# Performance work log

Hardware: AMD Instinct MI355X
Metric: run time of the kernel (lower is better)

## Reference

```python
import jax, jax.numpy as jnp
import numpy as np

T, M, D_IN, N = 4096, 512, 11, 51


def setup_inputs() -> dict:
    key = jax.random.key(0)
    ks = jax.random.split(key, 11)
    s = 1.0 / np.sqrt(N)  # torch LSTMCell/Linear default init scale
    return {
        "input": jax.random.normal(ks[0], (T, M, D_IN), dtype=jnp.float32),
        "W_ih1": jax.random.uniform(ks[1], (4 * N, D_IN), jnp.float32, -s, s),
        "W_hh1": jax.random.uniform(ks[2], (4 * N, N), jnp.float32, -s, s),
        "b_ih1": jax.random.uniform(ks[3], (4 * N,), jnp.float32, -s, s),
        "b_hh1": jax.random.uniform(ks[4], (4 * N,), jnp.float32, -s, s),
        "W_ih2": jax.random.uniform(ks[5], (4 * N, N), jnp.float32, -s, s),
        "W_hh2": jax.random.uniform(ks[6], (4 * N, N), jnp.float32, -s, s),
        "b_ih2": jax.random.uniform(ks[7], (4 * N,), jnp.float32, -s, s),
        "b_hh2": jax.random.uniform(ks[8], (4 * N,), jnp.float32, -s, s),
        "W_lin": jax.random.uniform(ks[9], (1, N), jnp.float32, -s, s),
        "b_lin": jax.random.uniform(ks[10], (1,), jnp.float32, -s, s),
        "future": 0,
    }


def _lstm_cell(x, h, c, W_ih, W_hh, b_ih, b_hh):
    # torch gate order: input, forget, cell(g), output
    gates = x @ W_ih.T + b_ih + h @ W_hh.T + b_hh  # [m, 4n]
    i, f, g, o = jnp.split(gates, 4, axis=-1)
    c_new = jax.nn.sigmoid(f) * c + jax.nn.sigmoid(i) * jnp.tanh(g)
    h_new = jax.nn.sigmoid(o) * jnp.tanh(c_new)
    return h_new, c_new


def reference(input, W_ih1, W_hh1, b_ih1, b_hh1, W_ih2, W_hh2, b_ih2, b_hh2,
              W_lin, b_lin, future):
    m = input.shape[1]
    n = W_hh1.shape[1]
    h1 = jnp.zeros((m, n), jnp.float32)
    c1 = jnp.zeros((m, n), jnp.float32)
    h2 = jnp.zeros((m, n), jnp.float32)
    c2 = jnp.zeros((m, n), jnp.float32)

    def step(carry, x_t):
        h1, c1, h2, c2 = carry
        h1, c1 = _lstm_cell(x_t, h1, c1, W_ih1, W_hh1, b_ih1, b_hh1)
        h2, c2 = _lstm_cell(h1, h2, c2, W_ih2, W_hh2, b_ih2, b_hh2)
        out = h2 @ W_lin.T + b_lin  # [m, 1]
        return (h1, c1, h2, c2), out

    _, outs = jax.lax.scan(step, (h1, c1, h2, c2), input)  # [T, m, 1]
    # torch.stack(outputs, 1).squeeze(2) -> [m, T]
    # (future loop is dimensionally invalid in the original for future>0; future=0)
    return outs[:, :, 0].T
```

## Files before the change

### kernel.cpp

```cpp
#include <hip/hip_runtime.h>

#define T_STEPS 4096
#define M_BATCH 512
#define D_INP   11
#define N_HID   51
#define G4      204

typedef float v4f __attribute__((ext_vector_type(4)));

__device__ __forceinline__ float tanh_fast(float v) {
    return 2.0f * __builtin_amdgcn_rcpf(1.0f + __expf(-2.0f * v)) - 1.0f;
}

__attribute__((amdgpu_waves_per_eu(2, 2)))
__global__ __launch_bounds__(256)
void lstm2_pipe2(const float* __restrict__ input,
                 const float* __restrict__ W_ih1, const float* __restrict__ W_hh1,
                 const float* __restrict__ b_ih1, const float* __restrict__ b_hh1,
                 const float* __restrict__ W_ih2, const float* __restrict__ W_hh2,
                 const float* __restrict__ b_ih2, const float* __restrict__ b_hh2,
                 const float* __restrict__ W_lin, const float* __restrict__ b_lin,
                 float* __restrict__ out)
{
    const int  tid = threadIdx.x;
    const int  col = blockIdx.x;
    const bool isg = tid < G4;
    const int  j   = isg ? tid : 0;

    __shared__ __align__(16) float hbuf[4][52];
    __shared__ __align__(16) float xs[2][64 * 12];
    __shared__ float act1[208];
    __shared__ float act2[208];
    __shared__ float outbuf[128];

    v4f wi1v[3], wh1v[13], wi2v[13], wh2v[13];
    #pragma unroll
    for (int i = 0; i < 3; ++i)
        #pragma unroll
        for (int e = 0; e < 4; ++e) {
            int k = i * 4 + e;
            wi1v[i][e] = (k < D_INP) ? W_ih1[j * D_INP + k] : 0.f;
        }
    #pragma unroll
    for (int i = 0; i < 13; ++i)
        #pragma unroll
        for (int e = 0; e < 4; ++e) {
            int k = i * 4 + e;
            float w1 = (k < N_HID) ? W_hh1[j * N_HID + k] : 0.f;
            float w2 = (k < N_HID) ? W_ih2[j * N_HID + k] : 0.f;
            float w3 = (k < N_HID) ? W_hh2[j * N_HID + k] : 0.f;
            wh1v[i][e] = w1; wi2v[i][e] = w2; wh2v[i][e] = w3;
        }
    const float bias1 = isg ? (b_ih1[j] + b_hh1[j]) : 0.f;
    const float bias2 = isg ? (b_ih2[j] + b_hh2[j]) : 0.f;
    const bool  gg = (j >= 2 * N_HID) && (j < 3 * N_HID);
    const float Sa = gg ? 2.f : 1.f, Aa = gg ? 2.f : 1.f, Ba = gg ? -1.f : 0.f;

    const int   u2   = tid - 64;
    const float wlin = (tid >= 64 && tid < 64 + N_HID) ? W_lin[u2] : 0.f;
    const float blin = b_lin[0];
    float c1 = 0.f, c2 = 0.f;

    if (tid < 208) (&hbuf[0][0])[tid] = 0.f;
    { float* xf = &xs[0][0];
      for (int i = tid; i < 2 * 64 * 12; i += 256) xf[i] = 0.f; }

    auto xload = [&](int c, int e) -> float {
        int s = e / 11, d = e - s * 11;
        int tc = c * 64 + s; if (tc > T_STEPS - 1) tc = T_STEPS - 1;
        return input[((size_t)tc * M_BATCH + col) * D_INP + d];
    };
    auto xput = [&](int buf, int e, float v) {
        int s = e / 11, d = e - s * 11;
        xs[buf][s * 12 + d] = v;
    };
    __syncthreads();

    {
        float v0 = xload(0, tid);
        float v1 = xload(0, tid + 256);
        float v2 = (tid < 192) ? xload(0, tid + 512) : 0.f;
        xput(0, tid, v0);
        xput(0, tid + 256, v1);
        if (tid < 192) xput(0, tid + 512, v2);
    }
    __syncthreads();

    float xr0 = 0.f, xr1 = 0.f, xr2 = 0.f;

    for (int t = 0; t <= T_STEPS; ++t) {
        if ((t & 63) == 0) {
            const int c = (t >> 6) + 1;
            xr0 = xload(c, tid);
            xr1 = xload(c, tid + 256);
            if (tid < 192) xr2 = xload(c, tid + 512);
        }
        if (isg) {
            const v4f* xp  = (const v4f*)&xs[(t >> 6) & 1][(t & 63) * 12];
            const v4f* h1p = (const v4f*)hbuf[(t + 1) & 1];
            const v4f* h2p = (const v4f*)hbuf[2 + (t & 1)];

            v4f a0 = xp[0] * wi1v[0];
            v4f a1 = xp[1] * wi1v[1];
            a0 += xp[2] * wi1v[2];
            v4f b0 = {0.f, 0.f, 0.f, 0.f}, b1 = {0.f, 0.f, 0.f, 0.f};
            #pragma unroll
            for (int i = 0; i < 13; ++i) {
                v4f h = h1p[i];
                if (i & 1) { a1 += h * wh1v[i]; b1 += h * wi2v[i]; }
                else       { a0 += h * wh1v[i]; b0 += h * wi2v[i]; }
            }
            #pragma unroll
            for (int i = 0; i < 13; ++i) {
                v4f h = h2p[i];
                if (i & 1) b1 += h * wh2v[i];
                else       b0 += h * wh2v[i];
            }
            v4f as = a0 + a1;
            float g1 = (as.x + as.y) + (as.z + as.w) + bias1;
            act1[j] = Aa * __builtin_amdgcn_rcpf(1.f + __expf(-Sa * g1)) + Ba;
            v4f bs = b0 + b1;
            float g2 = (bs.x + bs.y) + (bs.z + bs.w) + bias2;
            act2[j] = Aa * __builtin_amdgcn_rcpf(1.f + __expf(-Sa * g2)) + Ba;
        }
        __syncthreads();

        if (tid < N_HID) {
            float iv = act1[tid],             fv = act1[N_HID + tid];
            float gv = act1[2 * N_HID + tid], ov = act1[3 * N_HID + tid];
            c1 = fv * c1 + iv * gv;
            hbuf[t & 1][tid] = ov * tanh_fast(c1);
        }
        if (tid >= 64 && tid < 128) {
            float part = 0.f;
            if (u2 < N_HID && t >= 1) {
                float iv = act2[u2],             fv = act2[N_HID + u2];
                float gv = act2[2 * N_HID + u2], ov = act2[3 * N_HID + u2];
                c2 = fv * c2 + iv * gv;
                float h2v = ov * tanh_fast(c2);
                hbuf[2 + ((t - 1) & 1)][u2] = h2v;
                part = wlin * h2v;
            }
            #pragma unroll
            for (int off = 32; off > 0; off >>= 1)
                part += __shfl_down(part, off, 64);
            if (u2 == 0 && t >= 1) outbuf[(t - 1) & 127] = part + blin;
        }
        if ((t & 63) == 32) {
            const int buf = ((t >> 6) + 1) & 1;
            xput(buf, tid, xr0);
            xput(buf, tid + 256, xr1);
            if (tid < 192) xput(buf, tid + 512, xr2);
        }
        if ((t & 63) == 1 && t >= 65 && tid >= 128 && tid < 192) {
            const int tb = (t - 65) + (tid - 128);
            out[(size_t)col * T_STEPS + tb] = outbuf[tb & 127];
        }
        __syncthreads();
    }

    if (tid >= 128 && tid < 192) {
        const int idx = 4032 + (tid - 128);
        out[(size_t)col * T_STEPS + idx] = outbuf[idx & 127];
    }
}

extern "C" void kernel_launch(void* const* d_in, const int* in_sizes, int n_in,
                              void* d_out, int out_size, void* d_ws, size_t ws_size,
                              hipStream_t stream) {
    const float* input = (const float*)d_in[0];
    const float* W_ih1 = (const float*)d_in[1];
    const float* W_hh1 = (const float*)d_in[2];
    const float* b_ih1 = (const float*)d_in[3];
    const float* b_hh1 = (const float*)d_in[4];
    const float* W_ih2 = (const float*)d_in[5];
    const float* W_hh2 = (const float*)d_in[6];
    const float* b_ih2 = (const float*)d_in[7];
    const float* b_hh2 = (const float*)d_in[8];
    const float* W_lin = (const float*)d_in[9];
    const float* b_lin = (const float*)d_in[10];
    float* out = (float*)d_out;

    lstm2_pipe2<<<M_BATCH, 256, 0, stream>>>(
        input, W_ih1, W_hh1, b_ih1, b_hh1,
        W_ih2, W_hh2, b_ih2, b_hh2, W_lin, b_lin, out);
}
```

Baseline: 4.461 ms.

## Specialize waves per layer and keep all four gates per lane in registers

Each block now uses two waves, one per LSTM layer. Each lane holds the four gate weight rows for its hidden unit in 104 vector registers, so it computes the gate preactivations, activations and cell update itself. This removes the act1/act2 shared-memory round trip and one of the two barriers per timestep. The cost is much higher register pressure (waves_per_eu 1) and sequential work per lane across four gates, which lengthens the per-step critical path.

Measured after the change: 7.974 ms. 1.79x slower.

```diff
diff --git a/kernel.cpp b/kernel.cpp
--- a/kernel.cpp
+++ b/kernel.cpp
@@ -4,66 +4,85 @@
 #define M_BATCH 512
 #define D_INP   11
 #define N_HID   51
-#define G4      204
 
 typedef float v4f __attribute__((ext_vector_type(4)));
 
+__device__ __forceinline__ float sigmoid_fast(float v) {
+    return __builtin_amdgcn_rcpf(1.0f + __expf(-v));
+}
 __device__ __forceinline__ float tanh_fast(float v) {
     return 2.0f * __builtin_amdgcn_rcpf(1.0f + __expf(-2.0f * v)) - 1.0f;
 }
 
-__attribute__((amdgpu_waves_per_eu(2, 2)))
-__global__ __launch_bounds__(256)
-void lstm2_pipe2(const float* __restrict__ input,
-                 const float* __restrict__ W_ih1, const float* __restrict__ W_hh1,
-                 const float* __restrict__ b_ih1, const float* __restrict__ b_hh1,
-                 const float* __restrict__ W_ih2, const float* __restrict__ W_hh2,
-                 const float* __restrict__ b_ih2, const float* __restrict__ b_hh2,
-                 const float* __restrict__ W_lin, const float* __restrict__ b_lin,
-                 float* __restrict__ out)
+__attribute__((amdgpu_waves_per_eu(1, 1)))
+__global__ __launch_bounds__(128)
+void lstm2_wavespec(const float* __restrict__ input,
+                    const float* __restrict__ W_ih1, const float* __restrict__ W_hh1,
+                    const float* __restrict__ b_ih1, const float* __restrict__ b_hh1,
+                    const float* __restrict__ W_ih2, const float* __restrict__ W_hh2,
+                    const float* __restrict__ b_ih2, const float* __restrict__ b_hh2,
+                    const float* __restrict__ W_lin, const float* __restrict__ b_lin,
+                    float* __restrict__ out)
 {
-    const int  tid = threadIdx.x;
-    const int  col = blockIdx.x;
-    const bool isg = tid < G4;
-    const int  j   = isg ? tid : 0;
-
-    __shared__ __align__(16) float hbuf[4][52];
+    const int  tid  = threadIdx.x;
+    const int  col  = blockIdx.x;
+    const int  wid  = tid >> 6;
+    const int  lane = tid & 63;
+    const bool valid = lane < N_HID;
+
+    __shared__ __align__(16) float hbuf[2][52];
+    __shared__ __align__(16) float h2buf[52];
     __shared__ __align__(16) float xs[2][64 * 12];
-    __shared__ float act1[208];
-    __shared__ float act2[208];
     __shared__ float outbuf[128];
 
-    v4f wi1v[3], wh1v[13], wi2v[13], wh2v[13];
-    #pragma unroll
-    for (int i = 0; i < 3; ++i)
+    v4f   wv[104];
+    float bias[4];
+    float wlin = 0.f;
+    const float blin = b_lin[0];
+    float cstate = 0.f;
+
+    if (wid == 0) {
         #pragma unroll
-        for (int e = 0; e < 4; ++e) {
-            int k = i * 4 + e;
-            wi1v[i][e] = (k < D_INP) ? W_ih1[j * D_INP + k] : 0.f;
-        }
-    #pragma unroll
-    for (int i = 0; i < 13; ++i)
+        for (int q = 0; q < 4; ++q) {
+            const int r = q * N_HID + lane;
+            bias[q] = valid ? (b_ih1[r] + b_hh1[r]) : 0.f;
+            #pragma unroll
+            for (int i = 0; i < 3; ++i)
+                #pragma unroll
+                for (int e = 0; e < 4; ++e) {
+                    const int k = 4 * i + e;
+                    wv[i * 4 + q][e] = (valid && k < D_INP) ? W_ih1[r * D_INP + k] : 0.f;
+                }
+            #pragma unroll
+            for (int i = 3; i < 16; ++i)
+                #pragma unroll
+                for (int e = 0; e < 4; ++e) {
+                    const int k = 4 * (i - 3) + e;
+                    wv[i * 4 + q][e] = (valid && k < N_HID) ? W_hh1[r * N_HID + k] : 0.f;
+                }
+        }
+    } else {
         #pragma unroll
-        for (int e = 0; e < 4; ++e) {
-            int k = i * 4 + e;
-            float w1 = (k < N_HID) ? W_hh1[j * N_HID + k] : 0.f;
-            float w2 = (k < N_HID) ? W_ih2[j * N_HID + k] : 0.f;
-            float w3 = (k < N_HID) ? W_hh2[j * N_HID + k] : 0.f;
-            wh1v[i][e] = w1; wi2v[i][e] = w2; wh2v[i][e] = w3;
-        }
-    const float bias1 = isg ? (b_ih1[j] + b_hh1[j]) : 0.f;
-    const float bias2 = isg ? (b_ih2[j] + b_hh2[j]) : 0.f;
-    const bool  gg = (j >= 2 * N_HID) && (j < 3 * N_HID);
-    const float Sa = gg ? 2.f : 1.f, Aa = gg ? 2.f : 1.f, Ba = gg ? -1.f : 0.f;
-
-    const int   u2   = tid - 64;
-    const float wlin = (tid >= 64 && tid < 64 + N_HID) ? W_lin[u2] : 0.f;
-    const float blin = b_lin[0];
-    float c1 = 0.f, c2 = 0.f;
-
-    if (tid < 208) (&hbuf[0][0])[tid] = 0.f;
-    { float* xf = &xs[0][0];
-      for (int i = tid; i < 2 * 64 * 12; i += 256) xf[i] = 0.f; }
+        for (int q = 0; q < 4; ++q) {
+            const int r = q * N_HID + lane;
+            bias[q] = valid ? (b_ih2[r] + b_hh2[r]) : 0.f;
+            #pragma unroll
+            for (int i = 0; i < 13; ++i)
+                #pragma unroll
+                for (int e = 0; e < 4; ++e) {
+                    const int k = 4 * i + e;
+                    wv[i * 4 + q][e] = (valid && k < N_HID) ? W_ih2[r * N_HID + k] : 0.f;
+                }
+            #pragma unroll
+            for (int i = 13; i < 26; ++i)
+                #pragma unroll
+                for (int e = 0; e < 4; ++e) {
+                    const int k = 4 * (i - 13) + e;
+                    wv[i * 4 + q][e] = (valid && k < N_HID) ? W_hh2[r * N_HID + k] : 0.f;
+                }
+        }
+        wlin = valid ? W_lin[lane] : 0.f;
+    }
 
     auto xload = [&](int c, int e) -> float {
         int s = e / 11, d = e - s * 11;
@@ -74,93 +93,104 @@
         int s = e / 11, d = e - s * 11;
         xs[buf][s * 12 + d] = v;
     };
+
+    for (int i = tid; i < 2 * 52; i += 128) (&hbuf[0][0])[i] = 0.f;
+    for (int i = tid; i < 52;     i += 128) h2buf[i] = 0.f;
+    for (int i = tid; i < 2 * 64 * 12; i += 128) (&xs[0][0])[i] = 0.f;
     __syncthreads();
-
-    {
-        float v0 = xload(0, tid);
-        float v1 = xload(0, tid + 256);
-        float v2 = (tid < 192) ? xload(0, tid + 512) : 0.f;
-        xput(0, tid, v0);
-        xput(0, tid + 256, v1);
-        if (tid < 192) xput(0, tid + 512, v2);
+    #pragma unroll
+    for (int i = 0; i < 6; ++i) {
+        const int e = tid + 128 * i;
+        if (e < 704) xput(0, e, xload(0, e));
     }
     __syncthreads();
 
-    float xr0 = 0.f, xr1 = 0.f, xr2 = 0.f;
-
+    float xr[6];
+
+    #pragma unroll 1
     for (int t = 0; t <= T_STEPS; ++t) {
         if ((t & 63) == 0) {
             const int c = (t >> 6) + 1;
-            xr0 = xload(c, tid);
-            xr1 = xload(c, tid + 256);
-            if (tid < 192) xr2 = xload(c, tid + 512);
-        }
-        if (isg) {
-            const v4f* xp  = (const v4f*)&xs[(t >> 6) & 1][(t & 63) * 12];
-            const v4f* h1p = (const v4f*)hbuf[(t + 1) & 1];
-            const v4f* h2p = (const v4f*)hbuf[2 + (t & 1)];
-
-            v4f a0 = xp[0] * wi1v[0];
-            v4f a1 = xp[1] * wi1v[1];
-            a0 += xp[2] * wi1v[2];
-            v4f b0 = {0.f, 0.f, 0.f, 0.f}, b1 = {0.f, 0.f, 0.f, 0.f};
+            #pragma unroll
+            for (int i = 0; i < 6; ++i) {
+                const int e = tid + 128 * i;
+                xr[i] = (e < 704) ? xload(c, e) : 0.f;
+            }
+        }
+
+        const v4f* h1p = (const v4f*)hbuf[(t + 1) & 1];
+        v4f acc0 = {0.f,0.f,0.f,0.f}, acc1 = acc0, acc2 = acc0, acc3 = acc0;
+
+        if (wid == 0) {
+            const v4f* xp = (const v4f*)&xs[(t >> 6) & 1][(t & 63) * 12];
+            #pragma unroll
+            for (int i = 0; i < 3; ++i) {
+                const v4f v = xp[i];
+                acc0 += v * wv[i * 4 + 0]; acc1 += v * wv[i * 4 + 1];
+                acc2 += v * wv[i * 4 + 2]; acc3 += v * wv[i * 4 + 3];
+            }
+            #pragma unroll
+            for (int i = 3; i < 16; ++i) {
+                const v4f h = h1p[i - 3];
+                acc0 += h * wv[i * 4 + 0]; acc1 += h * wv[i * 4 + 1];
+                acc2 += h * wv[i * 4 + 2]; acc3 += h * wv[i * 4 + 3];
+            }
+        } else {
+            const v4f* h2p = (const v4f*)h2buf;
             #pragma unroll
             for (int i = 0; i < 13; ++i) {
-                v4f h = h1p[i];
-                if (i & 1) { a1 += h * wh1v[i]; b1 += h * wi2v[i]; }
-                else       { a0 += h * wh1v[i]; b0 += h * wi2v[i]; }
-            }
-            #pragma unroll
-            for (int i = 0; i < 13; ++i) {
-                v4f h = h2p[i];
-                if (i & 1) b1 += h * wh2v[i];
-                else       b0 += h * wh2v[i];
-            }
-            v4f as = a0 + a1;
-            float g1 = (as.x + as.y) + (as.z + as.w) + bias1;
-            act1[j] = Aa * __builtin_amdgcn_rcpf(1.f + __expf(-Sa * g1)) + Ba;
-            v4f bs = b0 + b1;
-            float g2 = (bs.x + bs.y) + (bs.z + bs.w) + bias2;
-            act2[j] = Aa * __builtin_amdgcn_rcpf(1.f + __expf(-Sa * g2)) + Ba;
-        }
-        __syncthreads();
-
-        if (tid < N_HID) {
-            float iv = act1[tid],             fv = act1[N_HID + tid];
-            float gv = act1[2 * N_HID + tid], ov = act1[3 * N_HID + tid];
-            c1 = fv * c1 + iv * gv;
-            hbuf[t & 1][tid] = ov * tanh_fast(c1);
-        }
-        if (tid >= 64 && tid < 128) {
-            float part = 0.f;
-            if (u2 < N_HID && t >= 1) {
-                float iv = act2[u2],             fv = act2[N_HID + u2];
-                float gv = act2[2 * N_HID + u2], ov = act2[3 * N_HID + u2];
-                c2 = fv * c2 + iv * gv;
-                float h2v = ov * tanh_fast(c2);
-                hbuf[2 + ((t - 1) & 1)][u2] = h2v;
-                part = wlin * h2v;
-            }
+                const v4f h = h1p[i];
+                acc0 += h * wv[i * 4 + 0]; acc1 += h * wv[i * 4 + 1];
+                acc2 += h * wv[i * 4 + 2]; acc3 += h * wv[i * 4 + 3];
+            }
+            #pragma unroll
+            for (int i = 13; i < 26; ++i) {
+                const v4f h = h2p[i - 13];
+                acc0 += h * wv[i * 4 + 0]; acc1 += h * wv[i * 4 + 1];
+                acc2 += h * wv[i * 4 + 2]; acc3 += h * wv[i * 4 + 3];
+            }
+        }
+
+        const float pre0 = (acc0.x + acc0.y) + (acc0.z + acc0.w) + bias[0];
+        const float pre1 = (acc1.x + acc1.y) + (acc1.z + acc1.w) + bias[1];
+        const float pre2 = (acc2.x + acc2.y) + (acc2.z + acc2.w) + bias[2];
+        const float pre3 = (acc3.x + acc3.y) + (acc3.z + acc3.w) + bias[3];
+        const float iv = sigmoid_fast(pre0);
+        const float fv = sigmoid_fast(pre1);
+        const float gv = tanh_fast(pre2);
+        const float ov = sigmoid_fast(pre3);
+        if (!(wid == 1 && t == 0))
+            cstate = fv * cstate + iv * gv;
+        const float hv = ov * tanh_fast(cstate);
+
+        if (wid == 0) {
+            if (valid) hbuf[t & 1][lane] = hv;
+            if ((t & 63) == 1 && t >= 65) {
+                const int tb = (t - 65) + lane;
+                out[(size_t)col * T_STEPS + tb] = outbuf[tb & 127];
+            }
+        } else {
+            if (valid && t >= 1) h2buf[lane] = hv;
+            float part = (t >= 1) ? wlin * hv : 0.f;
             #pragma unroll
             for (int off = 32; off > 0; off >>= 1)
                 part += __shfl_down(part, off, 64);
-            if (u2 == 0 && t >= 1) outbuf[(t - 1) & 127] = part + blin;
-        }
+            if (lane == 0 && t >= 1) outbuf[(t - 1) & 127] = part + blin;
+        }
+
         if ((t & 63) == 32) {
             const int buf = ((t >> 6) + 1) & 1;
-            xput(buf, tid, xr0);
-            xput(buf, tid + 256, xr1);
-            if (tid < 192) xput(buf, tid + 512, xr2);
-        }
-        if ((t & 63) == 1 && t >= 65 && tid >= 128 && tid < 192) {
-            const int tb = (t - 65) + (tid - 128);
-            out[(size_t)col * T_STEPS + tb] = outbuf[tb & 127];
+            #pragma unroll
+            for (int i = 0; i < 6; ++i) {
+                const int e = tid + 128 * i;
+                if (e < 704) xput(buf, e, xr[i]);
+            }
         }
         __syncthreads();
     }
 
-    if (tid >= 128 && tid < 192) {
-        const int idx = 4032 + (tid - 128);
+    if (wid == 0) {
+        const int idx = 4032 + lane;
         out[(size_t)col * T_STEPS + idx] = outbuf[idx & 127];
     }
 }
@@ -181,7 +211,7 @@
     const float* b_lin = (const float*)d_in[10];
     float* out = (float*)d_out;
 
-    lstm2_pipe2<<<M_BATCH, 256, 0, stream>>>(
+    lstm2_wavespec<<<M_BATCH, 128, 0, stream>>>(
         input, W_ih1, W_hh1, b_ih1, b_hh1,
         W_ih2, W_hh2, b_ih2, b_hh2, W_lin, b_lin, out);
 }
```
